# Performance work log

Measured on AMD Instinct MI355X. Metric: run time of the kernel, lower is better.

## Reference

```python
import jax, jax.numpy as jnp
import numpy as np

N_FILTERS = 10
# torch.linspace(2,100,10).to(int32) truncates toward zero
CELL_SIZES = np.linspace(2, 100, N_FILTERS).astype(np.int32)  # [2,12,23,34,45,56,67,78,89,100]
B, N = 16384, 4096


def setup_inputs() -> dict:
    key = jax.random.key(0)
    k1, k2, k3 = jax.random.split(key, 3)
    inp = jax.random.normal(k1, (B, N), dtype=jnp.float32)
    # DoA search grid in radians
    search_space = jax.random.uniform(k2, (N,), dtype=jnp.float32,
                                      minval=-jnp.pi / 2, maxval=jnp.pi / 2)
    w = jax.random.normal(k3, (1, N_FILTERS), dtype=jnp.float32) / 100 + 1.0 / N_FILTERS
    b = jnp.zeros((1,), dtype=jnp.float32)
    return {"inp": inp, "search_space": search_space, "w": w, "b": b}


def _top_peak(x):
    # vectorized replacement for the per-batch scipy.signal.find_peaks + sort:
    # a peak is a strict local max; pick the peak with the largest spectrum value.
    interior = (x[:, 1:-1] > x[:, :-2]) & (x[:, 1:-1] > x[:, 2:])  # [B, N-2]
    mask = jnp.pad(interior, ((0, 0), (1, 1)))                      # [B, N]
    scores = jnp.where(mask, x, -jnp.inf)
    return jnp.argmax(scores, axis=1)  # [B] int


def reference(inp, search_space, w, b):
    n = inp.shape[1]
    top1 = _top_peak(inp)  # [B], non-differentiable index
    outs = []
    for c in CELL_SIZES:
        c = int(c)
        offs = jnp.arange(-c, c)                       # [2c]
        idx = (top1[:, None] + offs[None, :]) % n      # [B, 2c] circular window
        vals = jnp.take_along_axis(inp, idx, axis=1)   # [B, 2c]
        sm = jax.nn.softmax(vals, axis=1)
        outs.append(jnp.sum(search_space[idx] * sm, axis=1))  # [B]
    feat = jnp.stack(outs, axis=1)                     # [B, 10]
    return jax.nn.relu(feat @ w.T + b)                 # [B, 1]
```

## Files before the change

kernel.cpp:

```cpp
#include <hip/hip_runtime.h>
#include <math.h>

#define N_COLS 4096
#define WIN 200
#define CENTER 100

__global__ __launch_bounds__(256) void filter_kernel(
    const float* __restrict__ inp,
    const float* __restrict__ ss,
    const float* __restrict__ w,
    const float* __restrict__ bias,
    float* __restrict__ out,
    int B)
{
    const int wave = threadIdx.x >> 6;
    const int lane = threadIdx.x & 63;
    const int row  = blockIdx.x * 4 + wave;
    if (row >= B) return;

    const float* __restrict__ x = inp + (size_t)row * N_COLS;

    float bestv = -INFINITY;
    int   besti = 0;

    #pragma unroll 4
    for (int k = 0; k < 16; ++k) {
        const int p = k * 256 + lane * 4;
        const float4 v = *reinterpret_cast<const float4*>(x + p);
        int li = p - 1;          if (li < 0) li = 0;
        int ri = p + 4;          if (ri > N_COLS - 1) ri = N_COLS - 1;
        const float left  = x[li];
        const float right = x[ri];

        if (p >= 1 && v.x > left && v.x > v.y) {
            if (v.x > bestv) { bestv = v.x; besti = p; }
        }
        if (v.y > v.x && v.y > v.z) {
            if (v.y > bestv) { bestv = v.y; besti = p + 1; }
        }
        if (v.z > v.y && v.z > v.w) {
            if (v.z > bestv) { bestv = v.z; besti = p + 2; }
        }
        if (p + 3 <= N_COLS - 2 && v.w > v.z && v.w > right) {
            if (v.w > bestv) { bestv = v.w; besti = p + 3; }
        }
    }

    #pragma unroll
    for (int off = 32; off >= 1; off >>= 1) {
        float ov = __shfl_xor(bestv, off, 64);
        int   oi = __shfl_xor(besti, off, 64);
        if (ov > bestv || (ov == bestv && oi < besti)) { bestv = ov; besti = oi; }
    }
    const int top1 = besti;

    float vv[4], sv[4];
    bool  valid[4];
    float lmax = -INFINITY;

    #pragma unroll
    for (int q = 0; q < 4; ++q) {
        const int j = lane + q * 64;
        valid[q] = (j < WIN);
        int pos = top1 - CENTER + j;
        if (pos < 0)        pos += N_COLS;
        if (pos >= N_COLS)  pos -= N_COLS;
        vv[q] = x[pos];
        sv[q] = ss[pos];
        if (valid[q] && vv[q] > lmax) lmax = vv[q];
    }
    #pragma unroll
    for (int off = 32; off >= 1; off >>= 1)
        lmax = fmaxf(lmax, __shfl_xor(lmax, off, 64));

    float e[4], t[4];
    #pragma unroll
    for (int q = 0; q < 4; ++q) {
        e[q] = valid[q] ? __expf(vv[q] - lmax) : 0.0f;
        t[q] = e[q] * sv[q];
    }

    const int cells[10] = {2, 12, 23, 34, 45, 56, 67, 78, 89, 100};
    float acc = 0.0f;
    #pragma unroll
    for (int f = 0; f < 10; ++f) {
        const int lo = CENTER - cells[f];
        const int hi = CENTER + cells[f];
        float s1 = 0.0f, s2 = 0.0f;
        #pragma unroll
        for (int q = 0; q < 4; ++q) {
            const int j = lane + q * 64;
            if (j >= lo && j < hi) { s1 += e[q]; s2 += t[q]; }
        }
        #pragma unroll
        for (int off = 32; off >= 1; off >>= 1) {
            s1 += __shfl_xor(s1, off, 64);
            s2 += __shfl_xor(s2, off, 64);
        }
        acc += (s2 / s1) * w[f];
    }

    if (lane == 0) {
        const float r = acc + bias[0];
        out[row] = r > 0.0f ? r : 0.0f;
    }
}

extern "C" void kernel_launch(void* const* d_in, const int* in_sizes, int n_in,
                              void* d_out, int out_size, void* d_ws, size_t ws_size,
                              hipStream_t stream) {
    const float* inp  = (const float*)d_in[0];
    const float* ss   = (const float*)d_in[1];
    const float* w    = (const float*)d_in[2];
    const float* bias = (const float*)d_in[3];
    float* out = (float*)d_out;

    const int B = in_sizes[0] / N_COLS;
    const int blocks = (B + 3) / 4;
    filter_kernel<<<blocks, 256, 0, stream>>>(inp, ss, w, bias, out, B);
}
```

Measured before the change: 361.1 us.

## Split each row across four waves with shuffle-based neighbor peaks

Each block now handles one row: each of the four waves loads its quarter of the row as float4s up front. Left and right neighbours come from lane shuffles and seam loads instead of extra scalar global loads. Per-wave peak results are combined through shared memory, and the ten filter reductions are spread across the waves. The softmax max-subtraction is dropped, which risks exp overflow for large inputs, and two block-wide barriers are added.

```diff
diff --git a/kernel.cpp b/kernel.cpp
--- a/kernel.cpp
+++ b/kernel.cpp
@@ -5,44 +5,55 @@
 #define WIN 200
 #define CENTER 100
 
-__global__ __launch_bounds__(256) void filter_kernel(
+__global__ __launch_bounds__(256, 4) void filter_kernel(
     const float* __restrict__ inp,
     const float* __restrict__ ss,
-    const float* __restrict__ w,
+    const float* __restrict__ wt,
     const float* __restrict__ bias,
     float* __restrict__ out,
     int B)
 {
     const int wave = threadIdx.x >> 6;
     const int lane = threadIdx.x & 63;
-    const int row  = blockIdx.x * 4 + wave;
+    const int row  = blockIdx.x;
     if (row >= B) return;
 
     const float* __restrict__ x = inp + (size_t)row * N_COLS;
 
+    __shared__ float s_bestv[4];
+    __shared__ int   s_besti[4];
+    __shared__ float s_acc[4];
+
+    const int base = wave * 1024;
+    float4 v[4];
+    #pragma unroll
+    for (int c = 0; c < 4; ++c)
+        v[c] = *reinterpret_cast<const float4*>(x + base + c * 256 + lane * 4);
+
+    float seamL = 0.0f, seamR = 0.0f;
+    if (lane == 0  && base > 0)               seamL = x[base - 1];
+    if (lane == 63 && base + 1024 < N_COLS)   seamR = x[base + 1024];
+
     float bestv = -INFINITY;
     int   besti = 0;
 
-    #pragma unroll 4
-    for (int k = 0; k < 16; ++k) {
-        const int p = k * 256 + lane * 4;
-        const float4 v = *reinterpret_cast<const float4*>(x + p);
-        int li = p - 1;          if (li < 0) li = 0;
-        int ri = p + 4;          if (ri > N_COLS - 1) ri = N_COLS - 1;
-        const float left  = x[li];
-        const float right = x[ri];
+    #pragma unroll
+    for (int c = 0; c < 4; ++c) {
+        const int p = base + c * 256 + lane * 4;
+        const float4 cc = v[c];
 
-        if (p >= 1 && v.x > left && v.x > v.y) {
-            if (v.x > bestv) { bestv = v.x; besti = p; }
-        }
-        if (v.y > v.x && v.y > v.z) {
-            if (v.y > bestv) { bestv = v.y; besti = p + 1; }
-        }
-        if (v.z > v.y && v.z > v.w) {
-            if (v.z > bestv) { bestv = v.z; besti = p + 2; }
-        }
-        if (p + 3 <= N_COLS - 2 && v.w > v.z && v.w > right) {
-            if (v.w > bestv) { bestv = v.w; besti = p + 3; }
+        float left  = __shfl_up(cc.w, 1, 64);
+        float right = __shfl_down(cc.x, 1, 64);
+        if (c > 0) { const float e0 = __shfl(v[c - 1].w, 63, 64); if (lane == 0)  left  = e0; }
+        else       { if (lane == 0)  left  = seamL; }
+        if (c < 3) { const float e1 = __shfl(v[c + 1].x, 0, 64);  if (lane == 63) right = e1; }
+        else       { if (lane == 63) right = seamR; }
+
+        if (p >= 1 && cc.x > left && cc.x > cc.y && cc.x > bestv) { bestv = cc.x; besti = p; }
+        if (cc.y > cc.x && cc.y > cc.z && cc.y > bestv)           { bestv = cc.y; besti = p + 1; }
+        if (cc.z > cc.y && cc.z > cc.w && cc.z > bestv)           { bestv = cc.z; besti = p + 2; }
+        if (p + 3 <= N_COLS - 2 && cc.w > cc.z && cc.w > right && cc.w > bestv) {
+            bestv = cc.w; besti = p + 3;
         }
     }
 
@@ -52,56 +63,55 @@
         int   oi = __shfl_xor(besti, off, 64);
         if (ov > bestv || (ov == bestv && oi < besti)) { bestv = ov; besti = oi; }
     }
-    const int top1 = besti;
+    if (lane == 0) { s_bestv[wave] = bestv; s_besti[wave] = besti; }
+    __syncthreads();
 
-    float vv[4], sv[4];
-    bool  valid[4];
-    float lmax = -INFINITY;
-
+    float bv = s_bestv[0]; int bi = s_besti[0];
     #pragma unroll
-    for (int q = 0; q < 4; ++q) {
-        const int j = lane + q * 64;
-        valid[q] = (j < WIN);
-        int pos = top1 - CENTER + j;
-        if (pos < 0)        pos += N_COLS;
-        if (pos >= N_COLS)  pos -= N_COLS;
-        vv[q] = x[pos];
-        sv[q] = ss[pos];
-        if (valid[q] && vv[q] > lmax) lmax = vv[q];
+    for (int k = 1; k < 4; ++k) {
+        const float ov = s_bestv[k]; const int oi = s_besti[k];
+        if (ov > bv || (ov == bv && oi < bi)) { bv = ov; bi = oi; }
     }
-    #pragma unroll
-    for (int off = 32; off >= 1; off >>= 1)
-        lmax = fmaxf(lmax, __shfl_xor(lmax, off, 64));
+    const int top1 = bi;
 
     float e[4], t[4];
     #pragma unroll
     for (int q = 0; q < 4; ++q) {
-        e[q] = valid[q] ? __expf(vv[q] - lmax) : 0.0f;
-        t[q] = e[q] * sv[q];
+        const int j = lane + q * 64;
+        const int pos = (top1 - CENTER + j) & (N_COLS - 1);
+        const float xv = x[pos];
+        const float sv = ss[pos];
+        e[q] = (j < WIN) ? __expf(xv) : 0.0f;
+        t[q] = e[q] * sv;
     }
 
-    const int cells[10] = {2, 12, 23, 34, 45, 56, 67, 78, 89, 100};
-    float acc = 0.0f;
+    float accw = 0.0f;
     #pragma unroll
-    for (int f = 0; f < 10; ++f) {
-        const int lo = CENTER - cells[f];
-        const int hi = CENTER + cells[f];
-        float s1 = 0.0f, s2 = 0.0f;
-        #pragma unroll
-        for (int q = 0; q < 4; ++q) {
-            const int j = lane + q * 64;
-            if (j >= lo && j < hi) { s1 += e[q]; s2 += t[q]; }
+    for (int i = 0; i < 3; ++i) {
+        const int f = wave + i * 4;
+        if (f < 10) {
+            const int cell = (18 + 98 * f) / 9;
+            const int lo = CENTER - cell;
+            const int hi = CENTER + cell;
+            float s1 = 0.0f, s2 = 0.0f;
+            #pragma unroll
+            for (int q = 0; q < 4; ++q) {
+                const int j = lane + q * 64;
+                if (j >= lo && j < hi) { s1 += e[q]; s2 += t[q]; }
+            }
+            #pragma unroll
+            for (int off = 32; off >= 1; off >>= 1) {
+                s1 += __shfl_xor(s1, off, 64);
+                s2 += __shfl_xor(s2, off, 64);
+            }
+            accw += (s2 / s1) * wt[f];
         }
-        #pragma unroll
-        for (int off = 32; off >= 1; off >>= 1) {
-            s1 += __shfl_xor(s1, off, 64);
-            s2 += __shfl_xor(s2, off, 64);
-        }
-        acc += (s2 / s1) * w[f];
     }
+    if (lane == 0) s_acc[wave] = accw;
+    __syncthreads();
 
-    if (lane == 0) {
-        const float r = acc + bias[0];
+    if (threadIdx.x == 0) {
+        const float r = s_acc[0] + s_acc[1] + s_acc[2] + s_acc[3] + bias[0];
         out[row] = r > 0.0f ? r : 0.0f;
     }
 }
@@ -111,11 +121,10 @@
                               hipStream_t stream) {
     const float* inp  = (const float*)d_in[0];
     const float* ss   = (const float*)d_in[1];
-    const float* w    = (const float*)d_in[2];
+    const float* wt   = (const float*)d_in[2];
     const float* bias = (const float*)d_in[3];
     float* out = (float*)d_out;
 
     const int B = in_sizes[0] / N_COLS;
-    const int blocks = (B + 3) / 4;
-    filter_kernel<<<blocks, 256, 0, stream>>>(inp, ss, w, bias, out, B);
+    filter_kernel<<<B, 256, 0, stream>>>(inp, ss, wt, bias, out, B);
 }
```

Measured after the change: 357.6 us, median of 2. About the same (-1.0%).
